# Optimization experiments

Measured on AMD Instinct MI355X. Metric: run time of the kernel, lower is better.

The kernel has to match this reference:

```python
import jax, jax.numpy as jnp
import numpy as np
from jax import lax

B, T = 8192, 2048
INIT_ALPHA = 0.1


def setup_inputs() -> dict:
    key = jax.random.key(0)
    kx, = jax.random.split(key, 1)
    # intermittent demand: small non-negative integers, many exact zeros
    x = jax.random.randint(kx, (B, T), 0, 3).astype(jnp.float32)
    alpha = jnp.full((1, 1), INIT_ALPHA, dtype=jnp.float32)  # learned smoothing weight
    Z0 = jnp.ones((B,), dtype=jnp.float32)  # demand-size state
    V0 = jnp.ones((B,), dtype=jnp.float32)  # inter-demand-interval state
    q0 = jnp.ones((B,), dtype=jnp.float32)  # periods since last nonzero demand
    return {"x": x, "alpha": alpha, "Z0": Z0, "V0": V0, "q0": q0}


def reference(x, alpha, Z0, V0, q0):
    """Croston's method recurrence (sba=False): out_t = Z_t / V_t.

    x: (B, T) demand series; states are per-series scalars carried through a scan.
    """
    a = alpha[0, 0]

    def step(carry, xt):  # xt: (B,)
        Z, V, q = carry
        Z_next = a * xt + (1.0 - a) * Z
        V_next = a * q + (1.0 - a) * V
        nz = xt != 0.0
        Z_next = jnp.where(nz, Z_next, Z)
        V_next = jnp.where(nz, V_next, V)
        q_next = jnp.where(nz, 1.0, q + 1.0)
        out = Z_next / V_next  # sba=False branch
        return (Z_next, V_next, q_next), out

    _, outs = lax.scan(step, (Z0, V0, q0), x.T)  # outs: (T, B)
    return outs.T  # (B, T)
```

## Files before the change

kernel.cpp:

```cpp
#include <hip/hip_runtime.h>


#define BSER 8192
#define TLEN 2048
#define CH   64
#define WARM 128
#define NCH  (TLEN / CH)
#define TW   32
#define LROW 33

__global__ __launch_bounds__(256) void croston_kernel(
    const float* __restrict__ x,
    const float* __restrict__ alpha,
    const float* __restrict__ Z0,
    const float* __restrict__ V0,
    const float* __restrict__ q0,
    float* __restrict__ out)
{
    __shared__ float lds_all[4][64 * LROW];

    const int warp = threadIdx.x >> 6;
    const int lane = threadIdx.x & 63;
    const int c    = blockIdx.x & (NCH - 1);
    const int sgq  = blockIdx.x >> 5;
    const int sg   = sgq * 4 + warp;
    const int sbase = sg * 64;
    const int s     = c * CH;
    float* lds = lds_all[warp];

    const float a  = alpha[0];
    const float ma = 1.0f - a;

    const int t_start = (s >= WARM) ? (s - WARM) : 0;
    float Z, V, q;
    if (t_start == 0) {
        Z = Z0[sbase + lane];
        V = V0[sbase + lane];
        q = q0[sbase + lane];
    } else {
        Z = 1.0f; V = 1.0f; q = 1.0f;
    }

    const int rbase = lane >> 3;
    const int col   = (lane & 7) * 4;

    for (int t0 = t_start; t0 < s + CH; t0 += TW) {
        #pragma unroll
        for (int i = 0; i < 8; ++i) {
            const int r = i * 8 + rbase;
            const float4 v4 = *(const float4*)(x + (size_t)(sbase + r) * TLEN + t0 + col);
            float* p = lds + r * LROW + col;
            p[0] = v4.x; p[1] = v4.y; p[2] = v4.z; p[3] = v4.w;
        }
        __syncthreads();

        const bool emit = (t0 >= s);

        float* myrow = lds + lane * LROW;
        #pragma unroll
        for (int j = 0; j < TW; ++j) {
            const float xt = myrow[j];
            const bool  nz = (xt != 0.0f);
            const float Zn = fmaf(ma, Z, a * xt);
            const float Vn = fmaf(ma, V, a * q);
            Z = nz ? Zn : Z;
            V = nz ? Vn : V;
            q = nz ? 1.0f : q + 1.0f;
            if (emit) myrow[j] = Z * __builtin_amdgcn_rcpf(V);
        }
        __syncthreads();

        if (emit) {
            #pragma unroll
            for (int i = 0; i < 8; ++i) {
                const int r = i * 8 + rbase;
                const float* p = lds + r * LROW + col;
                float4 v4;
                v4.x = p[0]; v4.y = p[1]; v4.z = p[2]; v4.w = p[3];
                *(float4*)(out + (size_t)(sbase + r) * TLEN + t0 + col) = v4;
            }
            __syncthreads();
        }
    }
}

extern "C" void kernel_launch(void* const* d_in, const int* in_sizes, int n_in,
                              void* d_out, int out_size, void* d_ws, size_t ws_size,
                              hipStream_t stream) {
    const float* x     = (const float*)d_in[0];
    const float* alpha = (const float*)d_in[1];
    const float* Z0    = (const float*)d_in[2];
    const float* V0    = (const float*)d_in[3];
    const float* q0    = (const float*)d_in[4];
    float* out = (float*)d_out;

    dim3 block(256);
    dim3 grid(32 * NCH);
    croston_kernel<<<grid, block, 0, stream>>>(x, alpha, Z0, V0, q0, out);
}
```

Measured before the change: 142.1 us.

## Replace LDS transpose staging with per-lane direct register loads and double buffering

Removes the shared-memory tile transpose and barriers; each lane loads its own series row with 16-byte vector loads into registers and scans them, with two register tiles so the next tile's loads are issued before the current scan. Waves are remapped so a block's waves cover consecutive time chunks of one series group. This trades LDS traffic and synchronisation for strided, less coalesced global loads and stores that rely on cache line reuse.

Result: no change. 143.0 us (+0.6%).

```diff
diff --git a/kernel.cpp b/kernel.cpp
--- a/kernel.cpp
+++ b/kernel.cpp
@@ -1,13 +1,13 @@
 #include <hip/hip_runtime.h>
 
 
-#define BSER 8192
 #define TLEN 2048
 #define CH   64
 #define WARM 128
 #define NCH  (TLEN / CH)
 #define TW   32
-#define LROW 33
+
+typedef float vf4 __attribute__((ext_vector_type(4)));
 
 __global__ __launch_bounds__(256) void croston_kernel(
     const float* __restrict__ x,
@@ -17,69 +17,85 @@
     const float* __restrict__ q0,
     float* __restrict__ out)
 {
-    __shared__ float lds_all[4][64 * LROW];
-
     const int warp = threadIdx.x >> 6;
     const int lane = threadIdx.x & 63;
-    const int c    = blockIdx.x & (NCH - 1);
-    const int sgq  = blockIdx.x >> 5;
-    const int sg   = sgq * 4 + warp;
-    const int sbase = sg * 64;
-    const int s     = c * CH;
-    float* lds = lds_all[warp];
+    const int w    = blockIdx.x * 4 + warp;
+    const int sg   = w >> 5;
+    const int c    = w & (NCH - 1);
+    const int series = sg * 64 + lane;
+    const int s      = c * CH;
 
     const float a  = alpha[0];
     const float ma = 1.0f - a;
 
+    const float* __restrict__ xr = x   + (size_t)series * TLEN;
+    float*       __restrict__ orow = out + (size_t)series * TLEN;
+
     const int t_start = (s >= WARM) ? (s - WARM) : 0;
     float Z, V, q;
     if (t_start == 0) {
-        Z = Z0[sbase + lane];
-        V = V0[sbase + lane];
-        q = q0[sbase + lane];
+        Z = Z0[series];
+        V = V0[series];
+        q = q0[series];
     } else {
         Z = 1.0f; V = 1.0f; q = 1.0f;
     }
 
-    const int rbase = lane >> 3;
-    const int col   = (lane & 7) * 4;
+    auto step = [&](float xt) {
+        const bool  nz = (xt != 0.0f);
+        const float Zn = fmaf(ma, Z, a * xt);
+        const float Vn = fmaf(ma, V, a * q);
+        Z = nz ? Zn : Z;
+        V = nz ? Vn : V;
+        q = nz ? 1.0f : q + 1.0f;
+    };
 
-    for (int t0 = t_start; t0 < s + CH; t0 += TW) {
+    auto ld_tile = [&](vf4* b, int t0) {
         #pragma unroll
-        for (int i = 0; i < 8; ++i) {
-            const int r = i * 8 + rbase;
-            const float4 v4 = *(const float4*)(x + (size_t)(sbase + r) * TLEN + t0 + col);
-            float* p = lds + r * LROW + col;
-            p[0] = v4.x; p[1] = v4.y; p[2] = v4.z; p[3] = v4.w;
-        }
-        __syncthreads();
+        for (int i = 0; i < 8; ++i)
+            b[i] = *(const vf4*)(xr + t0 + i * 4);
+    };
 
+    auto scan_tile = [&](vf4* b, int t0) {
         const bool emit = (t0 >= s);
-
-        float* myrow = lds + lane * LROW;
-        #pragma unroll
-        for (int j = 0; j < TW; ++j) {
-            const float xt = myrow[j];
-            const bool  nz = (xt != 0.0f);
-            const float Zn = fmaf(ma, Z, a * xt);
-            const float Vn = fmaf(ma, V, a * q);
-            Z = nz ? Zn : Z;
-            V = nz ? Vn : V;
-            q = nz ? 1.0f : q + 1.0f;
-            if (emit) myrow[j] = Z * __builtin_amdgcn_rcpf(V);
-        }
-        __syncthreads();
-
         if (emit) {
             #pragma unroll
             for (int i = 0; i < 8; ++i) {
-                const int r = i * 8 + rbase;
-                const float* p = lds + r * LROW + col;
-                float4 v4;
-                v4.x = p[0]; v4.y = p[1]; v4.z = p[2]; v4.w = p[3];
-                *(float4*)(out + (size_t)(sbase + r) * TLEN + t0 + col) = v4;
+                #pragma unroll
+                for (int k = 0; k < 4; ++k) {
+                    step(b[i][k]);
+                    b[i][k] = Z * __builtin_amdgcn_rcpf(V);
+                }
             }
-            __syncthreads();
+            #pragma unroll
+            for (int i = 0; i < 8; ++i)
+                *(vf4*)(orow + t0 + i * 4) = b[i];
+        } else {
+            #pragma unroll
+            for (int i = 0; i < 8; ++i) {
+                #pragma unroll
+                for (int k = 0; k < 4; ++k) step(b[i][k]);
+            }
+        }
+    };
+
+    const int t_end = s + CH;
+    vf4 A[8], B[8];
+    ld_tile(A, t_start);
+    ld_tile(B, t_start + TW);
+
+    for (int t0 = t_start; t0 < t_end; t0 += 2 * TW) {
+        if (t0 + 2 * TW < t_end) {
+            scan_tile(A, t0);
+            ld_tile(A, t0 + 2 * TW);
+        } else {
+            scan_tile(A, t0);
+        }
+        if (t0 + 3 * TW < t_end) {
+            scan_tile(B, t0 + TW);
+            ld_tile(B, t0 + 3 * TW);
+        } else {
+            scan_tile(B, t0 + TW);
         }
     }
 }
@@ -95,6 +111,6 @@
     float* out = (float*)d_out;
 
     dim3 block(256);
-    dim3 grid(32 * NCH);
+    dim3 grid(1024);
     croston_kernel<<<grid, block, 0, stream>>>(x, alpha, Z0, V0, q0, out);
 }
```

## Double-buffer input tiles via async global-to-LDS loads, drop block barriers

Applied to the files above, without the earlier changes.

Replaces the synchronous float4 load-to-LDS path with direct global_load_lds DMA into a two-slot per-wave ring. The next tiles are prefetched while the current one is processed, and s_waitcnt replaces __syncthreads. Blocks shrink to two waves with a remapped series/chunk grid, a rotated swizzle avoids LDS bank conflicts, and outputs use nontemporal stores. The aim is to hide global load latency behind the sequential recurrence. The cost is reliance on hand-written waitcnt ordering for correctness.

Result: faster. 130.0 us (-8.5%).

```diff
diff --git a/kernel.cpp b/kernel.cpp
--- a/kernel.cpp
+++ b/kernel.cpp
@@ -1,7 +1,7 @@
 #include <hip/hip_runtime.h>
+#include <stdint.h>
 
 
-#define BSER 8192
 #define TLEN 2048
 #define CH   64
 #define WARM 128
@@ -9,7 +9,14 @@
 #define TW   32
 #define LROW 33
 
-__global__ __launch_bounds__(256) void croston_kernel(
+typedef float vf4 __attribute__((ext_vector_type(4)));
+
+#define GLDS16(gp, lp)                                                        \
+    __builtin_amdgcn_global_load_lds(                                         \
+        (const __attribute__((address_space(1))) uint32_t*)(gp),              \
+        (__attribute__((address_space(3))) uint32_t*)(lp), 16, 0, 0)
+
+__global__ __launch_bounds__(128) void croston_kernel(
     const float* __restrict__ x,
     const float* __restrict__ alpha,
     const float* __restrict__ Z0,
@@ -17,21 +24,26 @@
     const float* __restrict__ q0,
     float* __restrict__ out)
 {
-    __shared__ float lds_all[4][64 * LROW];
+    __shared__ float ring[2][2][64 * TW];
+    __shared__ float outb[2][64 * LROW];
 
     const int warp = threadIdx.x >> 6;
     const int lane = threadIdx.x & 63;
-    const int c    = blockIdx.x & (NCH - 1);
-    const int sgq  = blockIdx.x >> 5;
-    const int sg   = sgq * 4 + warp;
+
+    const int xr = blockIdx.x & 7;
+    const int bm = blockIdx.x >> 3;
+    const int sg = xr * 16 + (bm & 15);
+    const int c  = (bm >> 4) * 2 + warp;
+
     const int sbase = sg * 64;
     const int s     = c * CH;
-    float* lds = lds_all[warp];
 
     const float a  = alpha[0];
     const float ma = 1.0f - a;
 
     const int t_start = (s >= WARM) ? (s - WARM) : 0;
+    const int ntiles  = (s + CH - t_start) / TW;
+
     float Z, V, q;
     if (t_start == 0) {
         Z = Z0[sbase + lane];
@@ -41,45 +53,79 @@
         Z = 1.0f; V = 1.0f; q = 1.0f;
     }
 
-    const int rbase = lane >> 3;
-    const int col   = (lane & 7) * 4;
+    const int rho  = lane >> 3;
+    const int kap  = lane & 7;
+    const int mrot = ((kap + rho) & 7) * 4;
 
-    for (int t0 = t_start; t0 < s + CH; t0 += TW) {
+    float* ring0 = ring[warp][0];
+    float* ring1 = ring[warp][1];
+    float* ob    = outb[warp];
+
+    auto dma_tile = [&](float* slot, int t0) {
+        const float* gbase = x + (size_t)(sbase + rho) * TLEN + t0 + mrot;
         #pragma unroll
-        for (int i = 0; i < 8; ++i) {
-            const int r = i * 8 + rbase;
-            const float4 v4 = *(const float4*)(x + (size_t)(sbase + r) * TLEN + t0 + col);
-            float* p = lds + r * LROW + col;
-            p[0] = v4.x; p[1] = v4.y; p[2] = v4.z; p[3] = v4.w;
-        }
-        __syncthreads();
+        for (int i = 0; i < 8; ++i)
+            GLDS16(gbase + (size_t)i * 8 * TLEN, slot + i * 256);
+    };
 
-        const bool emit = (t0 >= s);
+    auto step = [&](float xt) {
+        const bool  nz = (xt != 0.0f);
+        const float Zn = fmaf(ma, Z, a * xt);
+        const float Vn = fmaf(ma, V, a * q);
+        Z = nz ? Zn : Z;
+        V = nz ? Vn : V;
+        q = nz ? 1.0f : q + 1.0f;
+    };
 
-        float* myrow = lds + lane * LROW;
+    dma_tile(ring0, t_start);
+    dma_tile(ring1, t_start + TW);
+
+    const int srot = lane & 7;
+
+    for (int t = 0; t < ntiles; ++t) {
+        float* slot = (t & 1) ? ring1 : ring0;
+        const int t0 = t_start + t * TW;
+
+        asm volatile("s_waitcnt vmcnt(8)" ::: "memory");
+
+        vf4 v[8];
         #pragma unroll
-        for (int j = 0; j < TW; ++j) {
-            const float xt = myrow[j];
-            const bool  nz = (xt != 0.0f);
-            const float Zn = fmaf(ma, Z, a * xt);
-            const float Vn = fmaf(ma, V, a * q);
-            Z = nz ? Zn : Z;
-            V = nz ? Vn : V;
-            q = nz ? 1.0f : q + 1.0f;
-            if (emit) myrow[j] = Z * __builtin_amdgcn_rcpf(V);
-        }
-        __syncthreads();
+        for (int mm = 0; mm < 8; ++mm)
+            v[mm] = *(const vf4*)(slot + lane * 32 + (((mm - srot) & 7) << 2));
 
-        if (emit) {
+        asm volatile("s_waitcnt lgkmcnt(0)" ::: "memory");
+        if (t + 2 < ntiles) dma_tile(slot, t0 + 2 * TW);
+
+        if (t0 >= s) {
+            #pragma unroll
+            for (int mm = 0; mm < 8; ++mm) {
+                #pragma unroll
+                for (int k = 0; k < 4; ++k) {
+                    step(v[mm][k]);
+                    v[mm][k] = Z * __builtin_amdgcn_rcpf(V);
+                }
+            }
+            #pragma unroll
+            for (int mm = 0; mm < 8; ++mm) {
+                #pragma unroll
+                for (int k = 0; k < 4; ++k)
+                    ob[lane * LROW + 4 * mm + k] = v[mm][k];
+            }
+            asm volatile("s_waitcnt lgkmcnt(0)" ::: "memory");
             #pragma unroll
             for (int i = 0; i < 8; ++i) {
-                const int r = i * 8 + rbase;
-                const float* p = lds + r * LROW + col;
-                float4 v4;
-                v4.x = p[0]; v4.y = p[1]; v4.z = p[2]; v4.w = p[3];
-                *(float4*)(out + (size_t)(sbase + r) * TLEN + t0 + col) = v4;
+                const float* p = ob + (i * 8 + rho) * LROW + (kap << 2);
+                vf4 o4;
+                o4.x = p[0]; o4.y = p[1]; o4.z = p[2]; o4.w = p[3];
+                __builtin_nontemporal_store(
+                    o4, (vf4*)(out + (size_t)(sbase + i * 8 + rho) * TLEN + t0 + (kap << 2)));
             }
-            __syncthreads();
+        } else {
+            #pragma unroll
+            for (int mm = 0; mm < 8; ++mm) {
+                #pragma unroll
+                for (int k = 0; k < 4; ++k) step(v[mm][k]);
+            }
         }
     }
 }
@@ -94,7 +140,7 @@
     const float* q0    = (const float*)d_in[4];
     float* out = (float*)d_out;
 
-    dim3 block(256);
-    dim3 grid(32 * NCH);
+    dim3 block(128);
+    dim3 grid(2048);
     croston_kernel<<<grid, block, 0, stream>>>(x, alpha, Z0, V0, q0, out);
 }
```

## Halve chunk length, swizzle LDS, replace block barriers with wave-local waits

Applied to the files above, without the earlier changes.

Cuts each time chunk from 64 to 32 steps and the tile width from 32 to 16, giving 8192 independent wavefronts instead of 4096. Each wave now owns its own chunk rather than four waves sharing one chunk, and the block-level barriers become s_waitcnt lgkmcnt(0), since each wave uses only its private LDS slice. LDS uses a rotated-column swizzle with 16-byte vector reads and writes instead of a padded layout with scalar accesses, and the block index mapping is reordered. The shorter chunks mean the 128-step warm-up is a larger share of the total work, so recomputed steps increase in exchange for more parallelism and fewer synchronisation stalls.

Result: slower. 159.8 us (+12.5%).

```diff
diff --git a/kernel.cpp b/kernel.cpp
--- a/kernel.cpp
+++ b/kernel.cpp
@@ -1,15 +1,15 @@
 #include <hip/hip_runtime.h>
 
 
-#define BSER 8192
 #define TLEN 2048
-#define CH   64
+#define CH   32
 #define WARM 128
 #define NCH  (TLEN / CH)
-#define TW   32
-#define LROW 33
+#define TW   16
 
-__global__ __launch_bounds__(256) void croston_kernel(
+typedef float vf4 __attribute__((ext_vector_type(4)));
+
+__global__ __launch_bounds__(256, 8) void croston_kernel(
     const float* __restrict__ x,
     const float* __restrict__ alpha,
     const float* __restrict__ Z0,
@@ -17,21 +17,23 @@
     const float* __restrict__ q0,
     float* __restrict__ out)
 {
-    __shared__ float lds_all[4][64 * LROW];
+    __shared__ float lds_all[4][64 * TW];
 
     const int warp = threadIdx.x >> 6;
     const int lane = threadIdx.x & 63;
-    const int c    = blockIdx.x & (NCH - 1);
-    const int sgq  = blockIdx.x >> 5;
-    const int sg   = sgq * 4 + warp;
+
+    const int xr = blockIdx.x & 7;
+    const int m  = blockIdx.x >> 3;
+    const int sg = xr * 16 + (m >> 4);
+    const int c  = (m & 15) * 4 + warp;
+
     const int sbase = sg * 64;
     const int s     = c * CH;
-    float* lds = lds_all[warp];
+    const int t_start = (s >= WARM) ? (s - WARM) : 0;
 
     const float a  = alpha[0];
     const float ma = 1.0f - a;
 
-    const int t_start = (s >= WARM) ? (s - WARM) : 0;
     float Z, V, q;
     if (t_start == 0) {
         Z = Z0[sbase + lane];
@@ -41,45 +43,66 @@
         Z = 1.0f; V = 1.0f; q = 1.0f;
     }
 
-    const int rbase = lane >> 3;
-    const int col   = (lane & 7) * 4;
+    const int rsub = lane >> 2;
+    const int g    = lane & 3;
 
-    for (int t0 = t_start; t0 < s + CH; t0 += TW) {
+    float* lds   = lds_all[warp];
+    float* myrow = lds + lane * TW;
+
+    auto step = [&](float xt) {
+        const bool  nz = (xt != 0.0f);
+        const float Zn = fmaf(ma, Z, a * xt);
+        const float Vn = fmaf(ma, V, a * q);
+        Z = nz ? Zn : Z;
+        V = nz ? Vn : V;
+        q = nz ? 1.0f : q + 1.0f;
+    };
+    auto wsync = []() { asm volatile("s_waitcnt lgkmcnt(0)" ::: "memory"); };
+
+    const int t_end = s + CH;
+
+    for (int t0 = t_start; t0 < t_end; t0 += TW) {
         #pragma unroll
-        for (int i = 0; i < 8; ++i) {
-            const int r = i * 8 + rbase;
-            const float4 v4 = *(const float4*)(x + (size_t)(sbase + r) * TLEN + t0 + col);
-            float* p = lds + r * LROW + col;
-            p[0] = v4.x; p[1] = v4.y; p[2] = v4.z; p[3] = v4.w;
+        for (int i = 0; i < 4; ++i) {
+            const int row = i * 16 + rsub;
+            const vf4 v = *(const vf4*)(x + (size_t)(sbase + row) * TLEN + t0 + g * 4);
+            *(vf4*)(lds + row * TW + (((g + row) & 3) << 2)) = v;
         }
-        __syncthreads();
+        wsync();
+
+        vf4 vv[4];
+        #pragma unroll
+        for (int gg = 0; gg < 4; ++gg)
+            vv[gg] = *(const vf4*)(myrow + (((gg + lane) & 3) << 2));
+        wsync();
 
         const bool emit = (t0 >= s);
-
-        float* myrow = lds + lane * LROW;
-        #pragma unroll
-        for (int j = 0; j < TW; ++j) {
-            const float xt = myrow[j];
-            const bool  nz = (xt != 0.0f);
-            const float Zn = fmaf(ma, Z, a * xt);
-            const float Vn = fmaf(ma, V, a * q);
-            Z = nz ? Zn : Z;
-            V = nz ? Vn : V;
-            q = nz ? 1.0f : q + 1.0f;
-            if (emit) myrow[j] = Z * __builtin_amdgcn_rcpf(V);
-        }
-        __syncthreads();
-
         if (emit) {
             #pragma unroll
-            for (int i = 0; i < 8; ++i) {
-                const int r = i * 8 + rbase;
-                const float* p = lds + r * LROW + col;
-                float4 v4;
-                v4.x = p[0]; v4.y = p[1]; v4.z = p[2]; v4.w = p[3];
-                *(float4*)(out + (size_t)(sbase + r) * TLEN + t0 + col) = v4;
+            for (int gg = 0; gg < 4; ++gg) {
+                #pragma unroll
+                for (int k = 0; k < 4; ++k) {
+                    step(vv[gg][k]);
+                    vv[gg][k] = Z * __builtin_amdgcn_rcpf(V);
+                }
             }
-            __syncthreads();
+            #pragma unroll
+            for (int gg = 0; gg < 4; ++gg)
+                *(vf4*)(myrow + (((gg + lane) & 3) << 2)) = vv[gg];
+            wsync();
+            #pragma unroll
+            for (int i = 0; i < 4; ++i) {
+                const int row = i * 16 + rsub;
+                const vf4 o = *(const vf4*)(lds + row * TW + (((g + row) & 3) << 2));
+                *(vf4*)(out + (size_t)(sbase + row) * TLEN + t0 + g * 4) = o;
+            }
+            wsync();
+        } else {
+            #pragma unroll
+            for (int gg = 0; gg < 4; ++gg) {
+                #pragma unroll
+                for (int k = 0; k < 4; ++k) step(vv[gg][k]);
+            }
         }
     }
 }
@@ -95,6 +118,6 @@
     float* out = (float*)d_out;
 
     dim3 block(256);
-    dim3 grid(32 * NCH);
+    dim3 grid(2048);
     croston_kernel<<<grid, block, 0, stream>>>(x, alpha, Z0, V0, q0, out);
 }
```
